# Optimization experiments

Hardware: AMD Instinct MI355X
Metric: run time of the kernel (lower is better)

The kernel has to match this reference:

```python
import jax, jax.numpy as jnp
import numpy as np
import math

B, T, E = 2, 2048, 1024
D = 1024          # total inner dim (config.head_dim)
H = 16            # n_head
HD = D // H       # per-head dim = 64


def setup_inputs() -> dict:
    key = jax.random.key(0)
    k1, k2, k3, k4, k5 = jax.random.split(key, 5)
    s = 0.02
    return {
        "x": jax.random.normal(k1, (B, T, E), dtype=jnp.float32),
        "W_attn": jax.random.normal(k2, (E, 3 * D), dtype=jnp.float32) * s,
        "b_attn": jnp.zeros((3 * D,), dtype=jnp.float32),
        "W_proj": jax.random.normal(k3, (D, E), dtype=jnp.float32) * s,
        "b_proj": jnp.zeros((E,), dtype=jnp.float32),
    }


def reference(x, W_attn, b_attn, W_proj, b_proj):
    Bc, Tc, _ = x.shape
    qkv = x @ W_attn + b_attn                       # [B,T,3D]
    q, k, v = jnp.split(qkv, 3, axis=-1)            # each [B,T,D]
    # reshape to heads: [B,H,T,hd]
    q = q.reshape(Bc, Tc, H, HD).transpose(0, 2, 1, 3)
    k = k.reshape(Bc, Tc, H, HD).transpose(0, 2, 1, 3)
    v = v.reshape(Bc, Tc, H, HD).transpose(0, 2, 1, 3)
    scale = 1.0 / math.sqrt(HD)
    att = jnp.einsum("bhqd,bhkd->bhqk", q, k) * scale   # [B,H,T,T]
    causal = jnp.tril(jnp.ones((Tc, Tc), dtype=bool))
    att = jnp.where(causal[None, None], att, -jnp.inf)
    att = jax.nn.softmax(att, axis=-1)
    y = jnp.einsum("bhqk,bhkd->bhqd", att, v)           # [B,H,T,hd]
    y = y.transpose(0, 2, 1, 3).reshape(Bc, Tc, D)      # [B,T,D]
    return y @ W_proj + b_proj                          # [B,T,E]
```

## Files before the change

kernel.cpp:

```cpp
#include <hip/hip_runtime.h>

typedef unsigned short u16;
typedef unsigned char u8;
typedef signed char s8;
typedef unsigned int u32;
typedef short bf16x8 __attribute__((ext_vector_type(8)));
typedef float f32x4 __attribute__((ext_vector_type(4)));
typedef int i32x4 __attribute__((ext_vector_type(4)));

#define SXI 21.1666667f
#define SWI 1058.3333f
#define DEQ 4.4640015e-5f

__device__ __forceinline__ u16 f2bf(float f) {
  union { float f; u32 u; } v; v.f = f;
  u32 r = v.u + 0x7fffu + ((v.u >> 16) & 1u);
  return (u16)(r >> 16);
}
__device__ __forceinline__ u16 f2bf_fast(float f) {
  union { float f; u32 u; } v; v.f = f;
  return (u16)((v.u + 0x8000u) >> 16);
}
__device__ __forceinline__ s8 q8(float v, float s) {
  float x = fminf(127.f, fmaxf(-127.f, v * s));
  return (s8)__float2int_rn(x);
}
__device__ __forceinline__ float fexp2(float x) {
#if __has_builtin(__builtin_amdgcn_exp2f)
  return __builtin_amdgcn_exp2f(x);
#else
  return exp2f(x);
#endif
}

__device__ __forceinline__ void gld_lds16(const u16* g, u16* l) {
  __builtin_amdgcn_global_load_lds(
      (__attribute__((address_space(1))) u32*)(g),
      (__attribute__((address_space(3))) u32*)(l), 16, 0, 0);
}
__device__ __forceinline__ void gld_lds16b(const u8* g, u8* l) {
  __builtin_amdgcn_global_load_lds(
      (__attribute__((address_space(1))) u32*)(g),
      (__attribute__((address_space(3))) u32*)(l), 16, 0, 0);
}

__device__ __forceinline__ bf16x8 ldsfrag(const u16* base, int row, int c8) {
  return *(const bf16x8*)(base + row * 64 + ((c8 ^ (row & 7)) << 3));
}
__device__ __forceinline__ int swz4(int r) { return (r & 3) ^ ((r >> 2) & 3); }

template <int CTRL>
__device__ __forceinline__ float dppf(float x) {
  return __int_as_float(__builtin_amdgcn_update_dpp(0, __float_as_int(x), CTRL, 0xf, 0xf, true));
}
__device__ __forceinline__ float red16_max(float x) {
  x = fmaxf(x, dppf<0xB1>(x));
  x = fmaxf(x, dppf<0x4E>(x));
  x = fmaxf(x, dppf<0x141>(x));
  x = fmaxf(x, dppf<0x140>(x));
  return x;
}
__device__ __forceinline__ float red16_sum(float x) {
  x += dppf<0xB1>(x);
  x += dppf<0x4E>(x);
  x += dppf<0x141>(x);
  x += dppf<0x140>(x);
  return x;
}

__global__ __launch_bounds__(256) void k_prep(const float* __restrict__ x, u16* __restrict__ xb,
                                              s8* __restrict__ xq,
                                              const float* __restrict__ Wa, u16* __restrict__ WaT,
                                              s8* __restrict__ wq8,
                                              const float* __restrict__ Wp, u16* __restrict__ WpT) {
  __shared__ float t[64][65];
  const int id = blockIdx.x;
  if (id < 2048) {
    int i = (id * 256 + threadIdx.x) * 8;
    const float4* p = (const float4*)(x + i);
    float4 a = p[0], b = p[1];
    uint4 o;
    o.x = (u32)f2bf(a.x) | ((u32)f2bf(a.y) << 16);
    o.y = (u32)f2bf(a.z) | ((u32)f2bf(a.w) << 16);
    o.z = (u32)f2bf(b.x) | ((u32)f2bf(b.y) << 16);
    o.w = (u32)f2bf(b.z) | ((u32)f2bf(b.w) << 16);
    *(uint4*)(xb + i) = o;
    u32 lo = (u32)(u8)q8(a.x, SXI) | ((u32)(u8)q8(a.y, SXI) << 8) |
             ((u32)(u8)q8(a.z, SXI) << 16) | ((u32)(u8)q8(a.w, SXI) << 24);
    u32 hi = (u32)(u8)q8(b.x, SXI) | ((u32)(u8)q8(b.y, SXI) << 8) |
             ((u32)(u8)q8(b.z, SXI) << 16) | ((u32)(u8)q8(b.w, SXI) << 24);
    uint2 oq; oq.x = lo; oq.y = hi;
    *(uint2*)(xq + i) = oq;
  } else if (id < 2816) {
    int q = id - 2048;
    int bx = q % 48, by = q / 48;
    int c0 = bx * 64, r0 = by * 64;
    int tx = threadIdx.x & 63, ty = threadIdx.x >> 6;
#pragma unroll
    for (int i = ty; i < 64; i += 4) t[i][tx] = Wa[(size_t)(r0 + i) * 3072 + c0 + tx];
    __syncthreads();
#pragma unroll
    for (int i = ty; i < 64; i += 4) {
      int row = c0 + i;
      if (row < 2048)
        wq8[(size_t)row * 1024 + r0 + tx] = q8(t[tx][i], SWI);
      else
        WaT[(size_t)row * 1024 + r0 + tx] = f2bf(t[tx][i]);
    }
  } else {
    int q = id - 2816;
    int bx = q & 15, by = q >> 4;
    int c0 = bx * 64, r0 = by * 64;
    int tx = threadIdx.x & 63, ty = threadIdx.x >> 6;
#pragma unroll
    for (int i = ty; i < 64; i += 4) t[i][tx] = Wp[(size_t)(r0 + i) * 1024 + c0 + tx];
    __syncthreads();
#pragma unroll
    for (int i = ty; i < 64; i += 4)
      WpT[(size_t)(c0 + i) * 1024 + r0 + tx] = f2bf(t[tx][i]);
  }
}

__global__ __launch_bounds__(256) void k_gemm_qkv(const u16* __restrict__ xb,
                                                  const s8* __restrict__ xq,
                                                  const u16* __restrict__ Wt,
                                                  const s8* __restrict__ wq8,
                                                  const float* __restrict__ bias,
                                                  u16* __restrict__ qb, u16* __restrict__ kb,
                                                  u16* __restrict__ vtb) {
  const int id = blockIdx.x;
  const int tid = threadIdx.x;
  const int lane = tid & 63, w = tid >> 6;
  const int lr = lane & 15, lq = lane >> 4;

  if (id < 1024) {
    __shared__ __align__(16) u8 la8[64 * 64], lb8[128 * 64];
    const int wm = (w >> 1) << 5, wn = (w & 1) << 6;
    i32x4 acc[2][4];
#pragma unroll
    for (int mi = 0; mi < 2; ++mi)
#pragma unroll
      for (int ni = 0; ni < 4; ++ni) acc[mi][ni] = (i32x4){0, 0, 0, 0};
    const int m0 = (id >> 4) * 64, n0 = (id & 15) * 128;
    const int srow4 = tid >> 2;
    const int gcol4 = (((tid & 3) ^ swz4(srow4)) << 4);
    const u8* ag = (const u8*)xq + (size_t)(m0 + srow4) * 1024 + gcol4;
    const u8* bg = (const u8*)wq8 + (size_t)(n0 + srow4) * 1024 + gcol4;

    for (int k0 = 0; k0 < 1024; k0 += 64) {
      __syncthreads();
      gld_lds16b(ag + k0, la8 + (w * 16) * 64);
#pragma unroll
      for (int r = 0; r < 2; ++r)
        gld_lds16b(bg + (size_t)r * 64 * 1024 + k0, lb8 + (r * 64 + w * 16) * 64);
      __syncthreads();
      i32x4 a[2], b[4];
#pragma unroll
      for (int mi = 0; mi < 2; ++mi) {
        int m = wm + mi * 16 + lr;
        a[mi] = *(const i32x4*)(la8 + m * 64 + ((lq ^ swz4(m)) << 4));
      }
#pragma unroll
      for (int ni = 0; ni < 4; ++ni) {
        int n = wn + ni * 16 + lr;
        b[ni] = *(const i32x4*)(lb8 + n * 64 + ((lq ^ swz4(n)) << 4));
      }
#pragma unroll
      for (int mi = 0; mi < 2; ++mi)
#pragma unroll
        for (int ni = 0; ni < 4; ++ni)
          acc[mi][ni] = __builtin_amdgcn_mfma_i32_16x16x64_i8(a[mi], b[ni], acc[mi][ni], 0, 0, 0);
    }
#pragma unroll
    for (int mi = 0; mi < 2; ++mi) {
      int gm = m0 + wm + mi * 16 + lq * 4;
#pragma unroll
      for (int ni = 0; ni < 4; ++ni) {
        int gn = n0 + wn + ni * 16 + lr;
        float bv = bias[gn];
        int which = gn >> 10, head = (gn >> 6) & 15, hd = gn & 63;
#pragma unroll
        for (int r = 0; r < 4; ++r) {
          int row = gm + r;
          int b2 = row >> 11, tt = row & 2047;
          float v = (float)acc[mi][ni][r] * DEQ + bv;
          size_t bh = (size_t)(b2 * 16 + head);
          if (which == 0)
            qb[(bh * 2048 + tt) * 64 + hd] = f2bf(v * 0.18033688f);
          else
            kb[(bh * 2048 + tt) * 64 + hd] = f2bf(v);
        }
      }
    }
  } else {
    __shared__ u16 sA[64 * 64], sB[128 * 64];
    const int wm = (w >> 1) << 5, wn = (w & 1) << 6;
    f32x4 acc[2][4];
#pragma unroll
    for (int mi = 0; mi < 2; ++mi)
#pragma unroll
      for (int ni = 0; ni < 4; ++ni) acc[mi][ni] = (f32x4){0.f, 0.f, 0.f, 0.f};
    const int t2 = id - 1024;
    const int m0 = (t2 >> 5) * 64, n0 = (t2 & 31) * 128;
    const int srow = tid >> 3;
    const int gcol = ((tid & 7) ^ (srow & 7)) << 3;
    const u16* ag = Wt + 2048 * 1024 + (size_t)(m0 + srow) * 1024 + gcol;
    const u16* bg = xb + (size_t)(n0 + srow) * 1024 + gcol;
    u16* la = sA + w * 512;
    u16* lb = sB + w * 512;

    for (int k0 = 0; k0 < 1024; k0 += 64) {
      __syncthreads();
#pragma unroll
      for (int r = 0; r < 2; ++r) gld_lds16(ag + (size_t)r * 32 * 1024 + k0, la + r * 2048);
#pragma unroll
      for (int r = 0; r < 4; ++r) gld_lds16(bg + (size_t)r * 32 * 1024 + k0, lb + r * 2048);
      __syncthreads();
#pragma unroll
      for (int kk = 0; kk < 64; kk += 32) {
        const int c8 = (kk >> 3) + lq;
        bf16x8 af[2], bfr[4];
#pragma unroll
        for (int i = 0; i < 2; ++i) af[i] = ldsfrag(sA, wm + i * 16 + lr, c8);
#pragma unroll
        for (int i = 0; i < 4; ++i) bfr[i] = ldsfrag(sB, wn + i * 16 + lr, c8);
#pragma unroll
        for (int mi = 0; mi < 2; ++mi)
#pragma unroll
          for (int ni = 0; ni < 4; ++ni)
            acc[mi][ni] = __builtin_amdgcn_mfma_f32_16x16x32_bf16(af[mi], bfr[ni], acc[mi][ni], 0, 0, 0);
      }
    }
#pragma unroll
    for (int mi = 0; mi < 2; ++mi) {
      int gm = m0 + wm + mi * 16 + lq * 4;
      float4 bv = *(const float4*)(bias + 2048 + gm);
#pragma unroll
      for (int ni = 0; ni < 4; ++ni) {
        int gn = n0 + wn + ni * 16 + lr;
        int b = gn >> 11, tt = gn & 2047;
#pragma unroll
        for (int r = 0; r < 4; ++r) {
          int dv = gm + r;
          float v = acc[mi][ni][r] + ((const float*)&bv)[r];
          vtb[((size_t)(b * 1024 + dv)) * 2048 + tt] = f2bf(v);
        }
      }
    }
  }
}

__global__ __launch_bounds__(256, 4) void k_attn(const u16* __restrict__ qbp,
                                                 const u16* __restrict__ kbp,
                                                 const u16* __restrict__ vtp,
                                                 u16* __restrict__ yb,
                                                 float* __restrict__ po,
                                                 float* __restrict__ pml) {
  __shared__ u16 sK[2][64 * 64];
  __shared__ u16 sV[2][64 * 64];
  __shared__ u16 sP[64 * 64];

  const int tid = threadIdx.x;
  const int lane = tid & 63, w = tid >> 6;
  const int lr = lane & 15, lq = lane >> 4;
  const int l = blockIdx.x;
  const int bh = l & 31;
  const int u = l >> 5;
  const bool isX = (u < 16);
  const int p = isX ? u : (u - 16);
  const int NT = isX ? 17 : 16;
  const int pSw = isX ? p : -1;
  const int maskT = isX ? p : 15;
  const int kvY = 16 - p;

  const u16* qh = qbp + (size_t)bh * (2048 * 64);
  const u16* kh = kbp + (size_t)bh * (2048 * 64);
  const u16* vh = vtp + (size_t)bh * (64 * 2048);

  bf16x8 qa0, qa1, qb0, qb1;
  {
    const u16* qpb = qh + (size_t)(((31 - p) << 6) + w * 16 + lr) * 64 + lq * 8;
    qb0 = *(const bf16x8*)(qpb);
    qb1 = *(const bf16x8*)(qpb + 32);
    if (isX) {
      const u16* qpa = qh + (size_t)((p << 6) + w * 16 + lr) * 64 + lq * 8;
      qa0 = *(const bf16x8*)(qpa);
      qa1 = *(const bf16x8*)(qpa + 32);
    } else {
      qa0 = qb0; qa1 = qb1;
    }
  }

  const int srow = tid >> 3;
  const int gcol = ((tid & 7) ^ (srow & 7)) << 3;

  u16* pP[4][4];
#pragma unroll
  for (int nj = 0; nj < 4; ++nj) {
    int chunk = nj * 2 + (lr >> 3);
#pragma unroll
    for (int r = 0; r < 4; ++r) {
      int row = w * 16 + lq * 4 + r;
      pP[nj][r] = sP + row * 64 + ((chunk ^ (row & 7)) << 3) + (lr & 7);
    }
  }

  {
    const int kv0 = isX ? 0 : kvY;
    const int kv1 = isX ? ((1 <= p) ? 1 : 0) : (kvY + 1);
    u16* lk0 = sK[0] + w * 512;
    u16* lk1 = sK[1] + w * 512;
    u16* lv0 = sV[0] + w * 512;
#pragma unroll
    for (int r = 0; r < 2; ++r) {
      gld_lds16(kh + (size_t)(kv0 * 64 + r * 32 + srow) * 64 + gcol, lk0 + r * 2048);
      gld_lds16(vh + (size_t)(r * 32 + srow) * 2048 + kv0 * 64 + gcol, lv0 + r * 2048);
      gld_lds16(kh + (size_t)(kv1 * 64 + r * 32 + srow) * 64 + gcol, lk1 + r * 2048);
    }
  }
  __syncthreads();

  f32x4 s[4];
#pragma unroll
  for (int nj = 0; nj < 4; ++nj) s[nj] = (f32x4){0.f, 0.f, 0.f, 0.f};
  {
    bf16x8 q0 = (0 <= pSw) ? qa0 : qb0;
    bf16x8 q1 = (0 <= pSw) ? qa1 : qb1;
#pragma unroll
    for (int kk = 0; kk < 64; kk += 32) {
      const int c8 = (kk >> 3) + lq;
      bf16x8 kf[4];
#pragma unroll
      for (int nj = 0; nj < 4; ++nj) kf[nj] = ldsfrag(sK[0], nj * 16 + lr, c8);
#pragma unroll
      for (int nj = 0; nj < 4; ++nj)
        s[nj] = __builtin_amdgcn_mfma_f32_16x16x32_bf16(kk ? q1 : q0, kf[nj], s[nj], 0, 0, 0);
    }
  }

  f32x4 o[4];
  float mL2[4], lrp[4];
#pragma unroll
  for (int j = 0; j < 4; ++j) {
    o[j] = (f32x4){0.f, 0.f, 0.f, 0.f};
    mL2[j] = -1e30f;
    lrp[j] = 0.f;
  }

  const int b = bh >> 4, h = bh & 15;

  for (int t = 0; t < NT; ++t) {
    __syncthreads();

    if (t + 2 < NT) {
      int j = t + 2;
      int kv = isX ? ((j <= p) ? j : j - p - 1) : (kvY + j);
      u16* lk = sK[t & 1] + w * 512;
#pragma unroll
      for (int r = 0; r < 2; ++r)
        gld_lds16(kh + (size_t)(kv * 64 + r * 32 + srow) * 64 + gcol, lk + r * 2048);
    }
    if (t + 1 < NT) {
      int j = t + 1;
      int kv = isX ? ((j <= p) ? j : j - p - 1) : (kvY + j);
      u16* lv = sV[(t + 1) & 1] + w * 512;
#pragma unroll
      for (int r = 0; r < 2; ++r)
        gld_lds16(vh + (size_t)(r * 32 + srow) * 2048 + kv * 64 + gcol, lv + r * 2048);
    }

    f32x4 sn[4];
    if (t + 1 < NT) {
      const u16* nK = sK[(t + 1) & 1];
      bf16x8 q0 = (t + 1 <= pSw) ? qa0 : qb0;
      bf16x8 q1 = (t + 1 <= pSw) ? qa1 : qb1;
#pragma unroll
      for (int nj = 0; nj < 4; ++nj) sn[nj] = (f32x4){0.f, 0.f, 0.f, 0.f};
#pragma unroll
      for (int kk = 0; kk < 64; kk += 32) {
        const int c8 = (kk >> 3) + lq;
        bf16x8 kf[4];
#pragma unroll
        for (int nj = 0; nj < 4; ++nj) kf[nj] = ldsfrag(nK, nj * 16 + lr, c8);
#pragma unroll
        for (int nj = 0; nj < 4; ++nj)
          sn[nj] = __builtin_amdgcn_mfma_f32_16x16x32_bf16(kk ? q1 : q0, kf[nj], sn[nj], 0, 0, 0);
      }
    }

    if (t == maskT) {
      int rloc = w * 16 + lq * 4;
#pragma unroll
      for (int nj = 0; nj < 4; ++nj) {
        int cloc = nj * 16 + lr;
#pragma unroll
        for (int r = 0; r < 4; ++r)
          if (cloc > rloc + r) s[nj][r] = -1e30f;
      }
    }

    float mx[4];
#pragma unroll
    for (int r = 0; r < 4; ++r)
      mx[r] = red16_max(fmaxf(fmaxf(s[0][r], s[1][r]), fmaxf(s[2][r], s[3][r])));
    int need = 0;
#pragma unroll
    for (int r = 0; r < 4; ++r) need |= (mx[r] > mL2[r] + 8.f) ? 1 : 0;
    if (__any(need)) {
#pragma unroll
      for (int r = 0; r < 4; ++r) {
        float mn = fmaxf(mL2[r], mx[r]);
        float al = fexp2(mL2[r] - mn);
        mL2[r] = mn;
        lrp[r] *= al;
#pragma unroll
        for (int nj = 0; nj < 4; ++nj) o[nj][r] *= al;
      }
    }
#pragma unroll
    for (int nj = 0; nj < 4; ++nj)
#pragma unroll
      for (int r = 0; r < 4; ++r) {
        float pp = fexp2(s[nj][r] - mL2[r]);
        s[nj][r] = pp;
        lrp[r] += pp;
      }

#pragma unroll
    for (int nj = 0; nj < 4; ++nj)
#pragma unroll
      for (int r = 0; r < 4; ++r) *pP[nj][r] = f2bf_fast(s[nj][r]);
    asm volatile("s_waitcnt lgkmcnt(0)" ::: "memory");

    {
      const u16* cV = sV[t & 1];
#pragma unroll
      for (int kk = 0; kk < 64; kk += 32) {
        const int c8 = (kk >> 3) + lq;
        bf16x8 pa = ldsfrag(sP, w * 16 + lr, c8);
        bf16x8 vf[4];
#pragma unroll
        for (int nj = 0; nj < 4; ++nj) vf[nj] = ldsfrag(cV, nj * 16 + lr, c8);
#pragma unroll
        for (int nj = 0; nj < 4; ++nj)
          o[nj] = __builtin_amdgcn_mfma_f32_16x16x32_bf16(pa, vf[nj], o[nj], 0, 0, 0);
      }
    }

    if (isX && t == p) {
#pragma unroll
      for (int r = 0; r < 4; ++r) {
        float inv = 1.0f / red16_sum(lrp[r]);
        int row = (p << 6) + w * 16 + lq * 4 + r;
        size_t base = ((size_t)(b * 2048 + row)) * 1024 + h * 64;
#pragma unroll
        for (int nj = 0; nj < 4; ++nj) yb[base + nj * 16 + lr] = f2bf(o[nj][r] * inv);
      }
#pragma unroll
      for (int j = 0; j < 4; ++j) {
        o[j] = (f32x4){0.f, 0.f, 0.f, 0.f};
        mL2[j] = -1e30f;
        lrp[j] = 0.f;
      }
    }

    if (t + 1 < NT) {
#pragma unroll
      for (int nj = 0; nj < 4; ++nj) s[nj] = sn[nj];
    }
  }

  {
    const int pi = bh * 16 + p;
    const int S = isX ? 0 : 1;
    float* poo = po + (size_t)(pi * 2 + S) * 4096;
    float* pmm = pml + (size_t)(pi * 2 + S) * 128;
#pragma unroll
    for (int r = 0; r < 4; ++r) {
      float ls = red16_sum(lrp[r]);
      int row = w * 16 + lq * 4 + r;
      if (lr == 0) {
        pmm[row * 2] = mL2[r];
        pmm[row * 2 + 1] = ls;
      }
#pragma unroll
      for (int nj = 0; nj < 4; ++nj) poo[row * 64 + nj * 16 + lr] = o[nj][r];
    }
  }
}

__global__ __launch_bounds__(256) void k_merge(const float* __restrict__ po,
                                               const float* __restrict__ pml,
                                               u16* __restrict__ yb) {
  const int pi = blockIdx.x;
  const int bh = pi >> 4, p = pi & 15;
  const int b = bh >> 4, h = bh & 15;
  const int q0 = (31 - p) << 6;
  const float* oX = po + (size_t)(pi * 2 + 0) * 4096;
  const float* oY = po + (size_t)(pi * 2 + 1) * 4096;
  const float* mlX = pml + (size_t)(pi * 2 + 0) * 128;
  const float* mlY = pml + (size_t)(pi * 2 + 1) * 128;
#pragma unroll
  for (int k = 0; k < 16; ++k) {
    int idx = k * 256 + threadIdx.x;
    int row = idx >> 6, col = idx & 63;
    float mX = mlX[row * 2], lX = mlX[row * 2 + 1];
    float mY = mlY[row * 2], lY = mlY[row * 2 + 1];
    float m = fmaxf(mX, mY);
    float aX = fexp2(mX - m), aY = fexp2(mY - m);
    float linv = 1.0f / (lX * aX + lY * aY);
    float y = (oX[idx] * aX + oY[idx] * aY) * linv;
    yb[((size_t)(b * 2048 + q0 + row)) * 1024 + h * 64 + col] = f2bf(y);
  }
}

__global__ __launch_bounds__(256) void k_gemm_proj(const u16* __restrict__ ybuf,
                                                   const u16* __restrict__ Wt,
                                                   const float* __restrict__ bias,
                                                   float* __restrict__ out) {
  __shared__ u16 sA[64 * 64], sB[64 * 64];
  f32x4 acc[2][2];
#pragma unroll
  for (int mi = 0; mi < 2; ++mi)
#pragma unroll
    for (int ni = 0; ni < 2; ++ni) acc[mi][ni] = (f32x4){0.f, 0.f, 0.f, 0.f};

  const int m0 = blockIdx.y * 64, n0 = blockIdx.x * 64;
  const int tid = threadIdx.x;
  const int lane = tid & 63, w = tid >> 6;
  const int wm = (w >> 1) << 5, wn = (w & 1) << 5;
  const int lr = lane & 15, lq = lane >> 4;
  const int srow = tid >> 3;
  const int gcol = ((tid & 7) ^ (srow & 7)) << 3;
  const u16* ag = ybuf + (size_t)(m0 + srow) * 1024 + gcol;
  const u16* bg = Wt + (size_t)(n0 + srow) * 1024 + gcol;
  u16* la = sA + w * 512;
  u16* lb = sB + w * 512;

  for (int k0 = 0; k0 < 1024; k0 += 64) {
    __syncthreads();
#pragma unroll
    for (int r = 0; r < 2; ++r) {
      gld_lds16(ag + (size_t)r * 32 * 1024 + k0, la + r * 2048);
      gld_lds16(bg + (size_t)r * 32 * 1024 + k0, lb + r * 2048);
    }
    __syncthreads();
#pragma unroll
    for (int kk = 0; kk < 64; kk += 32) {
      const int c8 = (kk >> 3) + lq;
      bf16x8 af[2], bfr[2];
#pragma unroll
      for (int i = 0; i < 2; ++i) {
        af[i] = ldsfrag(sA, wm + i * 16 + lr, c8);
        bfr[i] = ldsfrag(sB, wn + i * 16 + lr, c8);
      }
#pragma unroll
      for (int mi = 0; mi < 2; ++mi)
#pragma unroll
        for (int ni = 0; ni < 2; ++ni)
          acc[mi][ni] = __builtin_amdgcn_mfma_f32_16x16x32_bf16(af[mi], bfr[ni], acc[mi][ni], 0, 0, 0);
    }
  }

#pragma unroll
  for (int mi = 0; mi < 2; ++mi) {
    int gm = m0 + wm + mi * 16 + lq * 4;
#pragma unroll
    for (int ni = 0; ni < 2; ++ni) {
      int gn = n0 + wn + ni * 16 + lr;
      float bv = bias[gn];
#pragma unroll
      for (int r = 0; r < 4; ++r) out[(size_t)(gm + r) * 1024 + gn] = acc[mi][ni][r] + bv;
    }
  }
}

extern "C" void kernel_launch(void* const* d_in, const int* in_sizes, int n_in,
                              void* d_out, int out_size, void* d_ws, size_t ws_size,
                              hipStream_t stream) {
  const float* x = (const float*)d_in[0];
  const float* W_attn = (const float*)d_in[1];
  const float* b_attn = (const float*)d_in[2];
  const float* W_proj = (const float*)d_in[3];
  const float* b_proj = (const float*)d_in[4];
  float* out = (float*)d_out;

  u16* ws = (u16*)d_ws;
  u16* xb = ws;
  u16* WaT = ws + 4194304;
  u16* qbuf = ws + 8388608;
  u16* kbuf = ws + 12582912;
  u16* vtb = ws + 16777216;
  u16* ybuf = ws + 20971520;
  s8* xq = (s8*)ybuf;
  s8* wq8 = (s8*)ybuf + 4194304;
  float* po = (float*)ws;
  float* pml = (float*)(ws + 25165824);
  u16* WpT = ws + 25427968;

  k_prep<<<dim3(3072), dim3(256), 0, stream>>>(x, xb, xq, W_attn, WaT, wq8, W_proj, WpT);
  k_gemm_qkv<<<dim3(1536), dim3(256), 0, stream>>>(xb, xq, WaT, wq8, b_attn, qbuf, kbuf, vtb);
  k_attn<<<dim3(1024), dim3(256), 0, stream>>>(qbuf, kbuf, vtb, ybuf, po, pml);
  k_merge<<<dim3(512), dim3(256), 0, stream>>>(po, pml, ybuf);
  k_gemm_proj<<<dim3(16, 64), dim3(256), 0, stream>>>(ybuf, WpT, b_proj, out);
}
```

Measured before the change: 175.2 us.

## Transpose attention MFMAs and keep P in registers via bpermute instead of LDS

Swaps the MFMA operand order so each lane holds scores for a single query row. Softmax max and sum then reduce across lanes with two shuffles instead of per-row DPP chains, and each lane tracks one running max and sum. The probability tile is packed to bf16 with v_cvt_pk_bf16_f32 and rearranged with ds_bpermute into the B operand of the PV MFMA. This removes the sP shared buffer, its LDS round trip and the waitcnt. Output and partial stores become vectorized. The cost is eight bpermutes plus selects per tile, and the register fragment layout is harder to get right.

```diff
diff --git a/kernel.cpp b/kernel.cpp
--- a/kernel.cpp
+++ b/kernel.cpp
@@ -17,10 +17,6 @@
   u32 r = v.u + 0x7fffu + ((v.u >> 16) & 1u);
   return (u16)(r >> 16);
 }
-__device__ __forceinline__ u16 f2bf_fast(float f) {
-  union { float f; u32 u; } v; v.f = f;
-  return (u16)((v.u + 0x8000u) >> 16);
-}
 __device__ __forceinline__ s8 q8(float v, float s) {
   float x = fminf(127.f, fmaxf(-127.f, v * s));
   return (s8)__float2int_rn(x);
@@ -32,6 +28,11 @@
   return exp2f(x);
 #endif
 }
+__device__ __forceinline__ u32 cvtpk_bf16(float lo, float hi) {
+  u32 r;
+  asm("v_cvt_pk_bf16_f32 %0, %1, %2" : "=v"(r) : "v"(lo), "v"(hi));
+  return r;
+}
 
 __device__ __forceinline__ void gld_lds16(const u16* g, u16* l) {
   __builtin_amdgcn_global_load_lds(
@@ -48,25 +49,6 @@
   return *(const bf16x8*)(base + row * 64 + ((c8 ^ (row & 7)) << 3));
 }
 __device__ __forceinline__ int swz4(int r) { return (r & 3) ^ ((r >> 2) & 3); }
-
-template <int CTRL>
-__device__ __forceinline__ float dppf(float x) {
-  return __int_as_float(__builtin_amdgcn_update_dpp(0, __float_as_int(x), CTRL, 0xf, 0xf, true));
-}
-__device__ __forceinline__ float red16_max(float x) {
-  x = fmaxf(x, dppf<0xB1>(x));
-  x = fmaxf(x, dppf<0x4E>(x));
-  x = fmaxf(x, dppf<0x141>(x));
-  x = fmaxf(x, dppf<0x140>(x));
-  return x;
-}
-__device__ __forceinline__ float red16_sum(float x) {
-  x += dppf<0xB1>(x);
-  x += dppf<0x4E>(x);
-  x += dppf<0x141>(x);
-  x += dppf<0x140>(x);
-  return x;
-}
 
 __global__ __launch_bounds__(256) void k_prep(const float* __restrict__ x, u16* __restrict__ xb,
                                               s8* __restrict__ xq,
@@ -258,7 +240,6 @@
                                                  float* __restrict__ pml) {
   __shared__ u16 sK[2][64 * 64];
   __shared__ u16 sV[2][64 * 64];
-  __shared__ u16 sP[64 * 64];
 
   const int tid = threadIdx.x;
   const int lane = tid & 63, w = tid >> 6;
@@ -294,16 +275,10 @@
   const int srow = tid >> 3;
   const int gcol = ((tid & 7) ^ (srow & 7)) << 3;
 
-  u16* pP[4][4];
-#pragma unroll
-  for (int nj = 0; nj < 4; ++nj) {
-    int chunk = nj * 2 + (lr >> 3);
-#pragma unroll
-    for (int r = 0; r < 4; ++r) {
-      int row = w * 16 + lq * 4 + r;
-      pP[nj][r] = sP + row * 64 + ((chunk ^ (row & 7)) << 3) + (lr & 7);
-    }
-  }
+  const int xadr0 = 4 * (lr + 16 * (2 * (lq & 1) + (lq >> 1)));
+  const int xadr1 = xadr0 ^ 64;
+  const bool bs0 = (lq & 1) != 0;
+  const bool bd1 = (lq >> 1) != 0;
 
   {
     const int kv0 = isX ? 0 : kvY;
@@ -334,20 +309,17 @@
       for (int nj = 0; nj < 4; ++nj) kf[nj] = ldsfrag(sK[0], nj * 16 + lr, c8);
 #pragma unroll
       for (int nj = 0; nj < 4; ++nj)
-        s[nj] = __builtin_amdgcn_mfma_f32_16x16x32_bf16(kk ? q1 : q0, kf[nj], s[nj], 0, 0, 0);
+        s[nj] = __builtin_amdgcn_mfma_f32_16x16x32_bf16(kf[nj], kk ? q1 : q0, s[nj], 0, 0, 0);
     }
   }
 
   f32x4 o[4];
-  float mL2[4], lrp[4];
-#pragma unroll
-  for (int j = 0; j < 4; ++j) {
-    o[j] = (f32x4){0.f, 0.f, 0.f, 0.f};
-    mL2[j] = -1e30f;
-    lrp[j] = 0.f;
-  }
+  float mL2 = -1e30f, lrp = 0.f;
+#pragma unroll
+  for (int j = 0; j < 4; ++j) o[j] = (f32x4){0.f, 0.f, 0.f, 0.f};
 
   const int b = bh >> 4, h = bh & 15;
+  const int qloc = w * 16 + lr;
 
   for (int t = 0; t < NT; ++t) {
     __syncthreads();
@@ -384,84 +356,116 @@
         for (int nj = 0; nj < 4; ++nj) kf[nj] = ldsfrag(nK, nj * 16 + lr, c8);
 #pragma unroll
         for (int nj = 0; nj < 4; ++nj)
-          sn[nj] = __builtin_amdgcn_mfma_f32_16x16x32_bf16(kk ? q1 : q0, kf[nj], sn[nj], 0, 0, 0);
+          sn[nj] = __builtin_amdgcn_mfma_f32_16x16x32_bf16(kf[nj], kk ? q1 : q0, sn[nj], 0, 0, 0);
       }
     }
 
     if (t == maskT) {
-      int rloc = w * 16 + lq * 4;
-#pragma unroll
-      for (int nj = 0; nj < 4; ++nj) {
-        int cloc = nj * 16 + lr;
+#pragma unroll
+      for (int nj = 0; nj < 4; ++nj)
 #pragma unroll
         for (int r = 0; r < 4; ++r)
-          if (cloc > rloc + r) s[nj][r] = -1e30f;
-      }
-    }
-
-    float mx[4];
-#pragma unroll
-    for (int r = 0; r < 4; ++r)
-      mx[r] = red16_max(fmaxf(fmaxf(s[0][r], s[1][r]), fmaxf(s[2][r], s[3][r])));
-    int need = 0;
-#pragma unroll
-    for (int r = 0; r < 4; ++r) need |= (mx[r] > mL2[r] + 8.f) ? 1 : 0;
-    if (__any(need)) {
+          if (nj * 16 + lq * 4 + r > qloc) s[nj][r] = -1e30f;
+    }
+
+    float mx = fmaxf(fmaxf(s[0][0], s[0][1]), fmaxf(s[0][2], s[0][3]));
+    mx = fmaxf(mx, fmaxf(fmaxf(s[1][0], s[1][1]), fmaxf(s[1][2], s[1][3])));
+    mx = fmaxf(mx, fmaxf(fmaxf(s[2][0], s[2][1]), fmaxf(s[2][2], s[2][3])));
+    mx = fmaxf(mx, fmaxf(fmaxf(s[3][0], s[3][1]), fmaxf(s[3][2], s[3][3])));
+    mx = fmaxf(mx, __shfl_xor(mx, 16));
+    mx = fmaxf(mx, __shfl_xor(mx, 32));
+    if (__any(mx > mL2 + 8.f)) {
+      float mn = fmaxf(mL2, mx);
+      float al = fexp2(mL2 - mn);
+      mL2 = mn;
+      lrp *= al;
+#pragma unroll
+      for (int nj = 0; nj < 4; ++nj)
+#pragma unroll
+        for (int r = 0; r < 4; ++r) o[nj][r] *= al;
+    }
+#pragma unroll
+    for (int nj = 0; nj < 4; ++nj)
 #pragma unroll
       for (int r = 0; r < 4; ++r) {
-        float mn = fmaxf(mL2[r], mx[r]);
-        float al = fexp2(mL2[r] - mn);
-        mL2[r] = mn;
-        lrp[r] *= al;
-#pragma unroll
-        for (int nj = 0; nj < 4; ++nj) o[nj][r] *= al;
-      }
-    }
-#pragma unroll
-    for (int nj = 0; nj < 4; ++nj)
-#pragma unroll
-      for (int r = 0; r < 4; ++r) {
-        float pp = fexp2(s[nj][r] - mL2[r]);
+        float pp = fexp2(s[nj][r] - mL2);
         s[nj][r] = pp;
-        lrp[r] += pp;
-      }
-
-#pragma unroll
-    for (int nj = 0; nj < 4; ++nj)
-#pragma unroll
-      for (int r = 0; r < 4; ++r) *pP[nj][r] = f2bf_fast(s[nj][r]);
-    asm volatile("s_waitcnt lgkmcnt(0)" ::: "memory");
+        lrp += pp;
+      }
+
+    u32 pk0[4], pk1[4];
+#pragma unroll
+    for (int nj = 0; nj < 4; ++nj) {
+      pk0[nj] = cvtpk_bf16(s[nj][0], s[nj][1]);
+      pk1[nj] = cvtpk_bf16(s[nj][2], s[nj][3]);
+    }
+
+    u32 W000, W001, W010, W011, W100, W101, W110, W111;
+    {
+      u32 v00 = bs0 ? pk0[1] : pk0[0];
+      u32 v01 = bs0 ? pk1[1] : pk1[0];
+      u32 v10 = bs0 ? pk0[0] : pk0[1];
+      u32 v11 = bs0 ? pk1[0] : pk1[1];
+      u32 r00 = (u32)__builtin_amdgcn_ds_bpermute(xadr0, (int)v00);
+      u32 r01 = (u32)__builtin_amdgcn_ds_bpermute(xadr0, (int)v01);
+      u32 r10 = (u32)__builtin_amdgcn_ds_bpermute(xadr1, (int)v10);
+      u32 r11 = (u32)__builtin_amdgcn_ds_bpermute(xadr1, (int)v11);
+      W000 = bd1 ? r10 : r00;
+      W001 = bd1 ? r11 : r01;
+      W010 = bd1 ? r00 : r10;
+      W011 = bd1 ? r01 : r11;
+      u32 u00 = bs0 ? pk0[3] : pk0[2];
+      u32 u01 = bs0 ? pk1[3] : pk1[2];
+      u32 u10 = bs0 ? pk0[2] : pk0[3];
+      u32 u11 = bs0 ? pk1[2] : pk1[3];
+      u32 t00 = (u32)__builtin_amdgcn_ds_bpermute(xadr0, (int)u00);
+      u32 t01 = (u32)__builtin_amdgcn_ds_bpermute(xadr0, (int)u01);
+      u32 t10 = (u32)__builtin_amdgcn_ds_bpermute(xadr1, (int)u10);
+      u32 t11 = (u32)__builtin_amdgcn_ds_bpermute(xadr1, (int)u11);
+      W100 = bd1 ? t10 : t00;
+      W101 = bd1 ? t11 : t01;
+      W110 = bd1 ? t00 : t10;
+      W111 = bd1 ? t01 : t11;
+    }
+    union B8 { u32 u[4]; bf16x8 v; };
+    B8 pb0u, pb1u;
+    pb0u.u[0] = W000; pb0u.u[1] = W001; pb0u.u[2] = W010; pb0u.u[3] = W011;
+    pb1u.u[0] = W100; pb1u.u[1] = W101; pb1u.u[2] = W110; pb1u.u[3] = W111;
 
     {
       const u16* cV = sV[t & 1];
 #pragma unroll
-      for (int kk = 0; kk < 64; kk += 32) {
-        const int c8 = (kk >> 3) + lq;
-        bf16x8 pa = ldsfrag(sP, w * 16 + lr, c8);
+      for (int kkidx = 0; kkidx < 2; ++kkidx) {
+        const int c8 = kkidx * 4 + lq;
+        bf16x8 pb = kkidx ? pb1u.v : pb0u.v;
         bf16x8 vf[4];
 #pragma unroll
         for (int nj = 0; nj < 4; ++nj) vf[nj] = ldsfrag(cV, nj * 16 + lr, c8);
 #pragma unroll
         for (int nj = 0; nj < 4; ++nj)
-          o[nj] = __builtin_amdgcn_mfma_f32_16x16x32_bf16(pa, vf[nj], o[nj], 0, 0, 0);
+          o[nj] = __builtin_amdgcn_mfma_f32_16x16x32_bf16(vf[nj], pb, o[nj], 0, 0, 0);
       }
     }
 
     if (isX && t == p) {
-#pragma unroll
-      for (int r = 0; r < 4; ++r) {
-        float inv = 1.0f / red16_sum(lrp[r]);
-        int row = (p << 6) + w * 16 + lq * 4 + r;
-        size_t base = ((size_t)(b * 2048 + row)) * 1024 + h * 64;
-#pragma unroll
-        for (int nj = 0; nj < 4; ++nj) yb[base + nj * 16 + lr] = f2bf(o[nj][r] * inv);
-      }
-#pragma unroll
-      for (int j = 0; j < 4; ++j) {
-        o[j] = (f32x4){0.f, 0.f, 0.f, 0.f};
-        mL2[j] = -1e30f;
-        lrp[j] = 0.f;
-      }
+      float ls = lrp;
+      ls += __shfl_xor(ls, 16);
+      ls += __shfl_xor(ls, 32);
+      float inv = 1.0f / ls;
+      size_t base = ((size_t)(b * 2048 + (p << 6) + qloc)) * 1024 + h * 64;
+#pragma unroll
+      for (int nj = 0; nj < 4; ++nj) {
+        ushort4 sv;
+        sv.x = f2bf(o[nj][0] * inv);
+        sv.y = f2bf(o[nj][1] * inv);
+        sv.z = f2bf(o[nj][2] * inv);
+        sv.w = f2bf(o[nj][3] * inv);
+        *(ushort4*)(yb + base + nj * 16 + lq * 4) = sv;
+      }
+#pragma unroll
+      for (int j = 0; j < 4; ++j) o[j] = (f32x4){0.f, 0.f, 0.f, 0.f};
+      mL2 = -1e30f;
+      lrp = 0.f;
     }
 
     if (t + 1 < NT) {
@@ -475,17 +479,16 @@
     const int S = isX ? 0 : 1;
     float* poo = po + (size_t)(pi * 2 + S) * 4096;
     float* pmm = pml + (size_t)(pi * 2 + S) * 128;
-#pragma unroll
-    for (int r = 0; r < 4; ++r) {
-      float ls = red16_sum(lrp[r]);
-      int row = w * 16 + lq * 4 + r;
-      if (lr == 0) {
-        pmm[row * 2] = mL2[r];
-        pmm[row * 2 + 1] = ls;
-      }
-#pragma unroll
-      for (int nj = 0; nj < 4; ++nj) poo[row * 64 + nj * 16 + lr] = o[nj][r];
-    }
+    float ls = lrp;
+    ls += __shfl_xor(ls, 16);
+    ls += __shfl_xor(ls, 32);
+    if (lq == 0) {
+      float2 ml; ml.x = mL2; ml.y = ls;
+      *(float2*)(pmm + qloc * 2) = ml;
+    }
+#pragma unroll
+    for (int nj = 0; nj < 4; ++nj)
+      *(f32x4*)(poo + qloc * 64 + nj * 16 + lq * 4) = o[nj];
   }
 }
 
```

After: 171.8 us. No clear change (-1.9%).
